# Kernel tuning notes

Hardware: AMD Instinct MI355X
Metric: run time of the kernel (lower is better)

The kernel has to match this reference:

```python
import jax, jax.numpy as jnp
import numpy as np

D = 1024
HEADS = 16
HD = D // HEADS


def setup_inputs() -> dict:
    key = jax.random.key(0)
    kx, kqkv, kout = jax.random.split(key, 3)
    x = jax.random.normal(kx, (2, 2048, D), dtype=jnp.float32)
    # torch Linear weight is [out, in]; store same layout
    W_qkv = jax.random.normal(kqkv, (3 * D, D), dtype=jnp.float32) * (D ** -0.5)
    W_out = jax.random.normal(kout, (D, D), dtype=jnp.float32) * (D ** -0.5)
    return {"x": x, "W_qkv": W_qkv, "W_out": W_out}


def reference(x, W_qkv, W_out):
    B, T, _ = x.shape
    scale = HD ** -0.5
    qkv = jnp.einsum('btd,ed->bte', x, W_qkv)            # [B,T,3D]
    qkv = qkv.reshape(B, T, 3, HEADS, HD)
    q = jnp.transpose(qkv[:, :, 0], (0, 2, 1, 3))        # [B,H,T,hd]
    k = jnp.transpose(qkv[:, :, 1], (0, 2, 1, 3))
    v = jnp.transpose(qkv[:, :, 2], (0, 2, 1, 3))
    attn = jnp.einsum('bhqd,bhkd->bhqk', q, k) * scale   # [B,H,T,T]
    causal = jnp.tril(jnp.ones((T, T), dtype=bool))
    attn = jnp.where(causal, attn, -jnp.inf)
    attn = jax.nn.softmax(attn, axis=-1)
    out = jnp.einsum('bhqk,bhkd->bhqd', attn, v)         # [B,H,T,hd]
    out = jnp.transpose(out, (0, 2, 1, 3)).reshape(B, T, HEADS * HD)
    return jnp.einsum('btd,ed->bte', out, W_out)
```

## Files before the change

### kernel.cpp

```cpp
#include <hip/hip_runtime.h>
#include <cmath>


typedef unsigned short u16;
typedef unsigned int u32;
typedef short short8 __attribute__((ext_vector_type(8)));
typedef float floatx4 __attribute__((ext_vector_type(4)));

#define T_SZ 2048
#define HD_SZ 64
#define QSCALE 0.1803368801111244f

__device__ __forceinline__ u16 f2bf(float f) {
  unsigned u = __float_as_uint(f);
  u += 0x7fffu + ((u >> 16) & 1u);
  return (u16)(u >> 16);
}

__device__ __forceinline__ u32 pack_bf2(float lo, float hi) {
  return __builtin_amdgcn_perm(__float_as_uint(hi), __float_as_uint(lo), 0x07060302u);
}

__device__ __forceinline__ void gload16(const u16* g, u16* l) {
  __builtin_amdgcn_global_load_lds(
      (const __attribute__((address_space(1))) void*)g,
      (__attribute__((address_space(3))) void*)l, 16, 0, 0);
}

__global__ __launch_bounds__(256) void cast3(const float* __restrict__ a, u16* __restrict__ ao, int na4,
                                             const float* __restrict__ b, u16* __restrict__ bo, int nb4,
                                             const float* __restrict__ c, u16* __restrict__ co, int nc4) {
  int i = blockIdx.x * 256 + threadIdx.x;
  const float* src;
  u16* dst;
  int j;
  if (i < na4) { src = a; dst = ao; j = i; }
  else if (i < na4 + nb4) { src = b; dst = bo; j = i - na4; }
  else { j = i - na4 - nb4; if (j >= nc4) return; src = c; dst = co; }
  float4 f = ((const float4*)src)[j];
  ushort4 o;
  o.x = f2bf(f.x); o.y = f2bf(f.y); o.z = f2bf(f.z); o.w = f2bf(f.w);
  ((ushort4*)dst)[j] = o;
}

__global__ __launch_bounds__(256, 3) void gemm_qkv(const u16* __restrict__ A,
                                                   const u16* __restrict__ Bt,
                                                   u16* __restrict__ Qf,
                                                   u16* __restrict__ Kf,
                                                   u16* __restrict__ Vf) {
  __shared__ u16 SM[2 * 128 * 64];
  u16* As = SM;
  u16* Bs = SM + 128 * 64;
  const int Kdim = 1024;
  const int tid = threadIdx.x;
  const int lane = tid & 63;
  const int wave = tid >> 6;
  const int quad = lane >> 4;
  const int l16 = lane & 15;
  const int wm = wave >> 1, wn = wave & 1;
  const int m0 = blockIdx.y * 128;
  const int n0 = blockIdx.x * 128;

  floatx4 acc[4][4];
#pragma unroll
  for (int i = 0; i < 4; i++)
#pragma unroll
    for (int j = 0; j < 4; j++) acc[i][j] = (floatx4){0.f, 0.f, 0.f, 0.f};

  const int srow = lane >> 3;
  const int scol = ((lane & 7) ^ srow) * 8;
  const u16* gpA[4];
  const u16* gpB[4];
  u16 *lpA[4], *lpB[4];
#pragma unroll
  for (int u = 0; u < 4; u++) {
    const int row = wave * 32 + u * 8 + srow;
    gpA[u] = A + (size_t)(m0 + row) * Kdim + scol;
    gpB[u] = Bt + (size_t)(n0 + row) * Kdim + scol;
    lpA[u] = As + (wave * 32 + u * 8) * 64 + lane * 8;
    lpB[u] = Bs + (wave * 32 + u * 8) * 64 + lane * 8;
  }

  const int fsw = l16 & 7;

  for (int k0 = 0; k0 < Kdim; k0 += 64) {
    __syncthreads();
#pragma unroll
    for (int u = 0; u < 4; u++) {
      gload16(gpA[u] + k0, lpA[u]);
      gload16(gpB[u] + k0, lpB[u]);
    }
    __syncthreads();

#pragma unroll
    for (int h = 0; h < 2; h++) {
      const int seg = ((h * 4 + quad) ^ fsw) * 8;
      short8 af[4], bf[4];
#pragma unroll
      for (int mt = 0; mt < 4; mt++)
        af[mt] = *(const short8*)&As[(wm * 64 + mt * 16 + l16) * 64 + seg];
#pragma unroll
      for (int nt = 0; nt < 4; nt++)
        bf[nt] = *(const short8*)&Bs[(wn * 64 + nt * 16 + l16) * 64 + seg];
#pragma unroll
      for (int mt = 0; mt < 4; mt++)
#pragma unroll
        for (int nt = 0; nt < 4; nt++)
          acc[mt][nt] = __builtin_amdgcn_mfma_f32_16x16x32_bf16(af[mt], bf[nt], acc[mt][nt], 0, 0, 0);
    }
  }

  const int dest = n0 >> 10;
  const int n0w = n0 + wn * 64;
  const int m_abs = m0 + wm * 64;
  const int b = m_abs >> 11;
  const int t0w = m_abs & 2047;
  const int h = (n0w >> 6) & 15;
  const int bh = b * 16 + h;
  u16* dstp = (dest == 0) ? Qf : (dest == 1) ? Kf : Vf;

  auto do_epi = [&](u16* ep) {
    if (dest == 2) {
#pragma unroll
      for (int nt = 0; nt < 4; nt++) {
#pragma unroll
        for (int mt = 0; mt < 4; mt++) {
          uint2 w;
          w.x = (u32)f2bf(acc[mt][nt][0]) | ((u32)f2bf(acc[mt][nt][1]) << 16);
          w.y = (u32)f2bf(acc[mt][nt][2]) | ((u32)f2bf(acc[mt][nt][3]) << 16);
          *(uint2*)&ep[(nt * 16 + l16) * 72 + mt * 16 + quad * 4] = w;
        }
      }
    } else {
      const float sc = (dest == 0) ? QSCALE : 1.0f;
#pragma unroll
      for (int mt = 0; mt < 4; mt++)
#pragma unroll
        for (int nt = 0; nt < 4; nt++)
#pragma unroll
          for (int r = 0; r < 4; r++)
            ep[(mt * 16 + quad * 4 + r) * 72 + nt * 16 + l16] =
                f2bf(acc[mt][nt][r] * sc);
    }
#pragma unroll
    for (int blk = 0; blk < 8; blk++) {
      const int tgd = blk >> 1;
      const int half = blk & 1;
      const short8 v = *(const short8*)&ep[(tgd * 16 + l16) * 72 + half * 32 + quad * 8];
      size_t base;
      if (dest == 0)
        base = ((size_t)(bh * 128 + (t0w >> 4) + tgd) * 2 + half) * 512;
      else
        base = (((size_t)(bh * 32 + (t0w >> 6)) * 4 + tgd) * 2 + half) * 512;
      *(short8*)(dstp + base + lane * 8) = v;
    }
  };

  __syncthreads();
  if (wave < 2) do_epi(&SM[wave * 64 * 72]);
  __syncthreads();
  if (wave >= 2) do_epi(&SM[(wave - 2) * 64 * 72]);
}

__global__ __launch_bounds__(256, 4) void gemm_out(const u16* __restrict__ A,
                                                   const u16* __restrict__ Bt,
                                                   float* __restrict__ Cout) {
  __shared__ u16 As[64 * 64];
  __shared__ u16 Bs[128 * 64];
  const int Kdim = 1024;
  const int tid = threadIdx.x;
  const int lane = tid & 63;
  const int wave = tid >> 6;
  const int quad = lane >> 4;
  const int l16 = lane & 15;
  const int wm = wave >> 1, wn = wave & 1;
  const int m0 = blockIdx.y * 64;
  const int n0 = blockIdx.x * 128;

  floatx4 acc[2][4];
#pragma unroll
  for (int i = 0; i < 2; i++)
#pragma unroll
    for (int j = 0; j < 4; j++) acc[i][j] = (floatx4){0.f, 0.f, 0.f, 0.f};

  const int srow = lane >> 3;
  const int scol = ((lane & 7) ^ srow) * 8;
  const u16* gpA[2];
  const u16* gpB[4];
  u16 *lpA[2], *lpB[4];
#pragma unroll
  for (int u = 0; u < 2; u++) {
    const int row = wave * 16 + u * 8 + srow;
    gpA[u] = A + (size_t)(m0 + row) * Kdim + scol;
    lpA[u] = As + (wave * 16 + u * 8) * 64 + lane * 8;
  }
#pragma unroll
  for (int u = 0; u < 4; u++) {
    const int row = wave * 32 + u * 8 + srow;
    gpB[u] = Bt + (size_t)(n0 + row) * Kdim + scol;
    lpB[u] = Bs + (wave * 32 + u * 8) * 64 + lane * 8;
  }

  const int fsw = l16 & 7;

  for (int k0 = 0; k0 < Kdim; k0 += 64) {
    __syncthreads();
#pragma unroll
    for (int u = 0; u < 2; u++) gload16(gpA[u] + k0, lpA[u]);
#pragma unroll
    for (int u = 0; u < 4; u++) gload16(gpB[u] + k0, lpB[u]);
    __syncthreads();

#pragma unroll
    for (int h = 0; h < 2; h++) {
      const int seg = ((h * 4 + quad) ^ fsw) * 8;
      short8 af[2], bf[4];
#pragma unroll
      for (int mt = 0; mt < 2; mt++)
        af[mt] = *(const short8*)&As[(wm * 32 + mt * 16 + l16) * 64 + seg];
#pragma unroll
      for (int nt = 0; nt < 4; nt++)
        bf[nt] = *(const short8*)&Bs[(wn * 64 + nt * 16 + l16) * 64 + seg];
#pragma unroll
      for (int mt = 0; mt < 2; mt++)
#pragma unroll
        for (int nt = 0; nt < 4; nt++)
          acc[mt][nt] = __builtin_amdgcn_mfma_f32_16x16x32_bf16(af[mt], bf[nt], acc[mt][nt], 0, 0, 0);
    }
  }

#pragma unroll
  for (int mt = 0; mt < 2; mt++)
#pragma unroll
    for (int nt = 0; nt < 4; nt++)
#pragma unroll
      for (int r = 0; r < 4; r++) {
        const int m = m0 + wm * 32 + mt * 16 + quad * 4 + r;
        const int n = n0 + wn * 64 + nt * 16 + l16;
        Cout[(size_t)m * 1024 + n] = acc[mt][nt][r];
      }
}

__global__ __launch_bounds__(256) void flash_attn(const u16* __restrict__ Qf,
                                                  const u16* __restrict__ Kf,
                                                  const u16* __restrict__ Vf,
                                                  u16* __restrict__ Og) {
  __shared__ u16 Ps[4][2][16 * 72];
  const int tid = threadIdx.x;
  const int lane = tid & 63, wave = tid >> 6;
  const int quad = lane >> 4, l16 = lane & 15;
  const int bh = blockIdx.x;
  const int py = blockIdx.y;
  const int p = (py < 8) ? py : 23 - py;
  const int gA = p, gB = 31 - p;
  const int b = bh >> 4, h = bh & 15;
  const u16* Qb = Qf + ((size_t)bh << 17);
  const u16* Kb = Kf + ((size_t)bh << 17);
  const u16* Vb = Vf + ((size_t)bh << 17);

  const u16* qpA = Qb + ((size_t)(gA * 4 + wave)) * 1024 + lane * 8;
  const u16* qpB = Qb + ((size_t)(gB * 4 + wave)) * 1024 + lane * 8;
  const short8 qfA0 = *(const short8*)qpA;
  const short8 qfA1 = *(const short8*)(qpA + 512);
  const short8 qfB0 = *(const short8*)qpB;
  const short8 qfB1 = *(const short8*)(qpB + 512);

  float lA = 0.f, lB = 0.f;
  floatx4 oA[4], oB[4];
#pragma unroll
  for (int dt = 0; dt < 4; dt++) {
    oA[dt] = (floatx4){0.f, 0.f, 0.f, 0.f};
    oB[dt] = (floatx4){0.f, 0.f, 0.f, 0.f};
  }
  u16* psA = &Ps[wave][0][0];
  u16* psB = &Ps[wave][1][0];

  short8 ka[4][2], va[4][2];

  auto stream_step = [&](bool diag, const short8& qf0, const short8& qf1,
                         floatx4* o_acc, float& l_sum, u16* ps) {
    floatx4 sacc[4];
#pragma unroll
    for (int nt = 0; nt < 4; nt++) {
      if (diag && nt > wave) continue;
      floatx4 s = (floatx4){0.f, 0.f, 0.f, 0.f};
      s = __builtin_amdgcn_mfma_f32_16x16x32_bf16(ka[nt][0], qf0, s, 0, 0, 0);
      s = __builtin_amdgcn_mfma_f32_16x16x32_bf16(ka[nt][1], qf1, s, 0, 0, 0);
      sacc[nt] = s;
    }
#pragma unroll
    for (int nt = 0; nt < 4; nt++) {
      float p0 = 0.f, p1 = 0.f, p2 = 0.f, p3 = 0.f;
      if (!(diag && nt > wave)) {
        p0 = exp2f(sacc[nt][0]);
        p1 = exp2f(sacc[nt][1]);
        p2 = exp2f(sacc[nt][2]);
        p3 = exp2f(sacc[nt][3]);
        if (diag && nt == wave) {
          if (quad * 4 + 0 > l16) p0 = 0.f;
          if (quad * 4 + 1 > l16) p1 = 0.f;
          if (quad * 4 + 2 > l16) p2 = 0.f;
          if (quad * 4 + 3 > l16) p3 = 0.f;
        }
        l_sum += (p0 + p1) + (p2 + p3);
      }
      uint2 w;
      w.x = pack_bf2(p0, p1);
      w.y = pack_bf2(p2, p3);
      *(uint2*)&ps[l16 * 72 + nt * 16 + quad * 4] = w;
    }
    const short8 pf0 = *(const short8*)&ps[l16 * 72 + quad * 8];
    const short8 pf1 = *(const short8*)&ps[l16 * 72 + 32 + quad * 8];
    const bool skip_hi = diag && (wave < 2);
#pragma unroll
    for (int dt = 0; dt < 4; dt++) {
      o_acc[dt] = __builtin_amdgcn_mfma_f32_16x16x32_bf16(va[dt][0], pf0, o_acc[dt], 0, 0, 0);
      if (!skip_hi)
        o_acc[dt] = __builtin_amdgcn_mfma_f32_16x16x32_bf16(va[dt][1], pf1, o_acc[dt], 0, 0, 0);
    }
  };

  for (int kt = 0; kt <= gB; kt++) {
    const u16* kp = Kb + (size_t)kt * 4096 + lane * 8;
    const u16* vp = Vb + (size_t)kt * 4096 + lane * 8;
#pragma unroll
    for (int nt = 0; nt < 4; nt++) {
      ka[nt][0] = *(const short8*)(kp + (nt * 2 + 0) * 512);
      ka[nt][1] = *(const short8*)(kp + (nt * 2 + 1) * 512);
    }
#pragma unroll
    for (int dt = 0; dt < 4; dt++) {
      va[dt][0] = *(const short8*)(vp + (dt * 2 + 0) * 512);
      va[dt][1] = *(const short8*)(vp + (dt * 2 + 1) * 512);
    }
    stream_step(kt == gB, qfB0, qfB1, oB, lB, psB);
    if (kt <= gA) stream_step(kt == gA, qfA0, qfA1, oA, lA, psA);
  }

  auto write_tile = [&](int g, floatx4* o_acc, float l_sum) {
    l_sum += __shfl_xor(l_sum, 16, 64);
    l_sum += __shfl_xor(l_sum, 32, 64);
    const float inv_l = 1.0f / l_sum;
    const int t0 = g * 64 + wave * 16;
    const size_t row = ((size_t)(b * 2048 + t0 + l16) << 10) + h * 64;
#pragma unroll
    for (int dt = 0; dt < 4; dt++) {
      uint2 w;
      w.x = pack_bf2(o_acc[dt][0] * inv_l, o_acc[dt][1] * inv_l);
      w.y = pack_bf2(o_acc[dt][2] * inv_l, o_acc[dt][3] * inv_l);
      *(uint2*)&Og[row + dt * 16 + quad * 4] = w;
    }
  };
  write_tile(gA, oA, lA);
  write_tile(gB, oB, lB);
}

extern "C" void kernel_launch(void* const* d_in, const int* in_sizes, int n_in,
                              void* d_out, int out_size, void* d_ws, size_t ws_size,
                              hipStream_t stream) {
  const float* x = (const float*)d_in[0];
  const float* Wqkv = (const float*)d_in[1];
  const float* Wout = (const float*)d_in[2];
  float* out = (float*)d_out;

  char* ws = (char*)d_ws;
  u16* xb    = (u16*)(ws + 0);
  u16* wqkvb = (u16*)(ws + 8388608);
  u16* woutb = (u16*)(ws + 14680064);
  u16* Qf    = (u16*)(ws + 16777216);
  u16* Kf    = (u16*)(ws + 25165824);
  u16* Vf    = (u16*)(ws + 33554432);
  u16* attn  = (u16*)(ws + 41943040);

  cast3<<<8192, 256, 0, stream>>>(x, xb, 1048576, Wqkv, wqkvb, 786432,
                                  Wout, woutb, 262144);

  gemm_qkv<<<dim3(24, 32), 256, 0, stream>>>(xb, wqkvb, Qf, Kf, Vf);

  flash_attn<<<dim3(32, 16), 256, 0, stream>>>(Qf, Kf, Vf, attn);

  gemm_out<<<dim3(8, 64), 256, 0, stream>>>(attn, woutb, out);
}
```

Before: 166.6 us.

## Split flash attention work across waves by key tiles with LDS reduction

Restructures the attention kernel so each wave handles a slice of the key dimension for all 64 query rows of a tile, rather than one 16-row query slice over all keys. Partial outputs and row sums are reduced across the four waves through shared memory before normalising and writing. The two query tiles are processed sequentially instead of interleaved, K/V are loaded once per wave per key tile, and launch bounds request two blocks per CU. This adds shared memory traffic, block-wide syncs and a cross-wave reduction epilogue, and raises register pressure from 16 output accumulators per wave.

```diff
diff --git a/kernel.cpp b/kernel.cpp
--- a/kernel.cpp
+++ b/kernel.cpp
@@ -241,118 +241,153 @@
       }
 }
 
-__global__ __launch_bounds__(256) void flash_attn(const u16* __restrict__ Qf,
-                                                  const u16* __restrict__ Kf,
-                                                  const u16* __restrict__ Vf,
-                                                  u16* __restrict__ Og) {
-  __shared__ u16 Ps[4][2][16 * 72];
+__global__ __launch_bounds__(256, 2) void flash_attn(const u16* __restrict__ Qf,
+                                                     const u16* __restrict__ Kf,
+                                                     const u16* __restrict__ Vf,
+                                                     u16* __restrict__ Og) {
+  __shared__ u16 Pq[4][4 * 16 * 40];
+  __shared__ float Osum[4][32 * 64];
+  __shared__ float Lsum[4][64];
   const int tid = threadIdx.x;
   const int lane = tid & 63, wave = tid >> 6;
   const int quad = lane >> 4, l16 = lane & 15;
   const int bh = blockIdx.x;
   const int py = blockIdx.y;
   const int p = (py < 8) ? py : 23 - py;
-  const int gA = p, gB = 31 - p;
   const int b = bh >> 4, h = bh & 15;
   const u16* Qb = Qf + ((size_t)bh << 17);
   const u16* Kb = Kf + ((size_t)bh << 17);
   const u16* Vb = Vf + ((size_t)bh << 17);
-
-  const u16* qpA = Qb + ((size_t)(gA * 4 + wave)) * 1024 + lane * 8;
-  const u16* qpB = Qb + ((size_t)(gB * 4 + wave)) * 1024 + lane * 8;
-  const short8 qfA0 = *(const short8*)qpA;
-  const short8 qfA1 = *(const short8*)(qpA + 512);
-  const short8 qfB0 = *(const short8*)qpB;
-  const short8 qfB1 = *(const short8*)(qpB + 512);
-
-  float lA = 0.f, lB = 0.f;
-  floatx4 oA[4], oB[4];
-#pragma unroll
-  for (int dt = 0; dt < 4; dt++) {
-    oA[dt] = (floatx4){0.f, 0.f, 0.f, 0.f};
-    oB[dt] = (floatx4){0.f, 0.f, 0.f, 0.f};
-  }
-  u16* psA = &Ps[wave][0][0];
-  u16* psB = &Ps[wave][1][0];
-
-  short8 ka[4][2], va[4][2];
-
-  auto stream_step = [&](bool diag, const short8& qf0, const short8& qf1,
-                         floatx4* o_acc, float& l_sum, u16* ps) {
-    floatx4 sacc[4];
-#pragma unroll
-    for (int nt = 0; nt < 4; nt++) {
-      if (diag && nt > wave) continue;
-      floatx4 s = (floatx4){0.f, 0.f, 0.f, 0.f};
-      s = __builtin_amdgcn_mfma_f32_16x16x32_bf16(ka[nt][0], qf0, s, 0, 0, 0);
-      s = __builtin_amdgcn_mfma_f32_16x16x32_bf16(ka[nt][1], qf1, s, 0, 0, 0);
-      sacc[nt] = s;
-    }
-#pragma unroll
-    for (int nt = 0; nt < 4; nt++) {
-      float p0 = 0.f, p1 = 0.f, p2 = 0.f, p3 = 0.f;
-      if (!(diag && nt > wave)) {
-        p0 = exp2f(sacc[nt][0]);
-        p1 = exp2f(sacc[nt][1]);
-        p2 = exp2f(sacc[nt][2]);
-        p3 = exp2f(sacc[nt][3]);
-        if (diag && nt == wave) {
-          if (quad * 4 + 0 > l16) p0 = 0.f;
-          if (quad * 4 + 1 > l16) p1 = 0.f;
-          if (quad * 4 + 2 > l16) p2 = 0.f;
-          if (quad * 4 + 3 > l16) p3 = 0.f;
+  u16* pq = &Pq[wave][0];
+
+  const int gs[2] = {p, 31 - p};
+
+  for (int ph = 0; ph < 2; ph++) {
+    const int g = gs[ph];
+
+    short8 qf[4][2];
+#pragma unroll
+    for (int qg = 0; qg < 4; qg++) {
+      const u16* qp = Qb + ((size_t)(g * 4 + qg)) * 1024 + lane * 8;
+      qf[qg][0] = *(const short8*)qp;
+      qf[qg][1] = *(const short8*)(qp + 512);
+    }
+
+    float l_part[4] = {0.f, 0.f, 0.f, 0.f};
+    floatx4 o[4][4];
+#pragma unroll
+    for (int dt = 0; dt < 4; dt++)
+#pragma unroll
+      for (int qg = 0; qg < 4; qg++) o[dt][qg] = (floatx4){0.f, 0.f, 0.f, 0.f};
+
+    auto process_kt = [&](int kt, int par, bool diag) {
+      const u16* kb = Kb + ((size_t)(kt * 4 + wave) * 2) * 512 + lane * 8;
+      const short8 ka0 = *(const short8*)kb;
+      const short8 ka1 = *(const short8*)(kb + 512);
+#pragma unroll
+      for (int qg = 0; qg < 4; qg++) {
+        uint2 w;
+        if (diag && wave > qg) {
+          w.x = 0u; w.y = 0u;
+        } else {
+          floatx4 s = (floatx4){0.f, 0.f, 0.f, 0.f};
+          s = __builtin_amdgcn_mfma_f32_16x16x32_bf16(ka0, qf[qg][0], s, 0, 0, 0);
+          s = __builtin_amdgcn_mfma_f32_16x16x32_bf16(ka1, qf[qg][1], s, 0, 0, 0);
+          float p0 = exp2f(s[0]);
+          float p1 = exp2f(s[1]);
+          float p2 = exp2f(s[2]);
+          float p3 = exp2f(s[3]);
+          if (diag && wave == qg) {
+            if (quad * 4 + 0 > l16) p0 = 0.f;
+            if (quad * 4 + 1 > l16) p1 = 0.f;
+            if (quad * 4 + 2 > l16) p2 = 0.f;
+            if (quad * 4 + 3 > l16) p3 = 0.f;
+          }
+          l_part[qg] += (p0 + p1) + (p2 + p3);
+          w.x = pack_bf2(p0, p1);
+          w.y = pack_bf2(p2, p3);
         }
-        l_sum += (p0 + p1) + (p2 + p3);
-      }
-      uint2 w;
-      w.x = pack_bf2(p0, p1);
-      w.y = pack_bf2(p2, p3);
-      *(uint2*)&ps[l16 * 72 + nt * 16 + quad * 4] = w;
-    }
-    const short8 pf0 = *(const short8*)&ps[l16 * 72 + quad * 8];
-    const short8 pf1 = *(const short8*)&ps[l16 * 72 + 32 + quad * 8];
-    const bool skip_hi = diag && (wave < 2);
-#pragma unroll
-    for (int dt = 0; dt < 4; dt++) {
-      o_acc[dt] = __builtin_amdgcn_mfma_f32_16x16x32_bf16(va[dt][0], pf0, o_acc[dt], 0, 0, 0);
-      if (!skip_hi)
-        o_acc[dt] = __builtin_amdgcn_mfma_f32_16x16x32_bf16(va[dt][1], pf1, o_acc[dt], 0, 0, 0);
-    }
-  };
-
-  for (int kt = 0; kt <= gB; kt++) {
-    const u16* kp = Kb + (size_t)kt * 4096 + lane * 8;
-    const u16* vp = Vb + (size_t)kt * 4096 + lane * 8;
-#pragma unroll
-    for (int nt = 0; nt < 4; nt++) {
-      ka[nt][0] = *(const short8*)(kp + (nt * 2 + 0) * 512);
-      ka[nt][1] = *(const short8*)(kp + (nt * 2 + 1) * 512);
-    }
-#pragma unroll
-    for (int dt = 0; dt < 4; dt++) {
-      va[dt][0] = *(const short8*)(vp + (dt * 2 + 0) * 512);
-      va[dt][1] = *(const short8*)(vp + (dt * 2 + 1) * 512);
-    }
-    stream_step(kt == gB, qfB0, qfB1, oB, lB, psB);
-    if (kt <= gA) stream_step(kt == gA, qfA0, qfA1, oA, lA, psA);
-  }
-
-  auto write_tile = [&](int g, floatx4* o_acc, float l_sum) {
-    l_sum += __shfl_xor(l_sum, 16, 64);
-    l_sum += __shfl_xor(l_sum, 32, 64);
-    const float inv_l = 1.0f / l_sum;
-    const int t0 = g * 64 + wave * 16;
-    const size_t row = ((size_t)(b * 2048 + t0 + l16) << 10) + h * 64;
-#pragma unroll
-    for (int dt = 0; dt < 4; dt++) {
-      uint2 w;
-      w.x = pack_bf2(o_acc[dt][0] * inv_l, o_acc[dt][1] * inv_l);
-      w.y = pack_bf2(o_acc[dt][2] * inv_l, o_acc[dt][3] * inv_l);
-      *(uint2*)&Og[row + dt * 16 + quad * 4] = w;
-    }
-  };
-  write_tile(gA, oA, lA);
-  write_tile(gB, oB, lB);
+        *(uint2*)&pq[(qg * 16 + l16) * 40 + par * 16 + quad * 4] = w;
+      }
+    };
+
+    const int npair = (g >> 1) + 1;
+    for (int ktp = 0; ktp < npair; ktp++) {
+      const int kt0 = ktp * 2;
+      const int kt1 = kt0 + 1;
+      const bool has1 = (kt1 <= g);
+
+      process_kt(kt0, 0, kt0 == g);
+      if (has1) {
+        process_kt(kt1, 1, kt1 == g);
+      } else {
+        const uint2 z = {0u, 0u};
+#pragma unroll
+        for (int qg = 0; qg < 4; qg++)
+          *(uint2*)&pq[(qg * 16 + l16) * 40 + 16 + quad * 4] = z;
+      }
+
+      short8 pf[4];
+#pragma unroll
+      for (int qg = 0; qg < 4; qg++)
+        pf[qg] = *(const short8*)&pq[(qg * 16 + l16) * 40 + quad * 8];
+
+      const int ktv = (quad < 2) ? kt0 : (has1 ? kt1 : kt0);
+      const int vl = ((wave & 1) * 2 + (quad & 1)) * 16 + l16;
+#pragma unroll
+      for (int dt = 0; dt < 4; dt++) {
+        const u16* vsrc = Vb + ((size_t)((ktv * 4 + dt) * 2 + (wave >> 1))) * 512 + vl * 8;
+        const short8 va = *(const short8*)vsrc;
+#pragma unroll
+        for (int qg = 0; qg < 4; qg++)
+          o[dt][qg] = __builtin_amdgcn_mfma_f32_16x16x32_bf16(va, pf[qg], o[dt][qg], 0, 0, 0);
+      }
+    }
+
+#pragma unroll
+    for (int qg = 0; qg < 4; qg++) {
+      l_part[qg] += __shfl_xor(l_part[qg], 16, 64);
+      l_part[qg] += __shfl_xor(l_part[qg], 32, 64);
+    }
+    if (quad == 0) {
+#pragma unroll
+      for (int qg = 0; qg < 4; qg++) Lsum[wave][qg * 16 + l16] = l_part[qg];
+    }
+
+    float linv[4];
+    for (int c = 0; c < 2; c++) {
+#pragma unroll
+      for (int dtl = 0; dtl < 2; dtl++) {
+        const int dt = c * 2 + dtl;
+#pragma unroll
+        for (int qg = 0; qg < 4; qg++)
+#pragma unroll
+          for (int r = 0; r < 4; r++)
+            Osum[wave][(dtl * 16 + quad * 4 + r) * 64 + qg * 16 + l16] = o[dt][qg][r];
+      }
+      __syncthreads();
+      if (c == 0) {
+#pragma unroll
+        for (int qg = 0; qg < 4; qg++)
+          linv[qg] = 1.0f / (Lsum[0][qg * 16 + l16] + Lsum[1][qg * 16 + l16] +
+                             Lsum[2][qg * 16 + l16] + Lsum[3][qg * 16 + l16]);
+      }
+      const int ld0 = wave * 8 + quad * 2;
+#pragma unroll
+      for (int qg = 0; qg < 4; qg++) {
+        const int qrow = qg * 16 + l16;
+        float v0 = Osum[0][(ld0 + 0) * 64 + qrow] + Osum[1][(ld0 + 0) * 64 + qrow] +
+                   Osum[2][(ld0 + 0) * 64 + qrow] + Osum[3][(ld0 + 0) * 64 + qrow];
+        float v1 = Osum[0][(ld0 + 1) * 64 + qrow] + Osum[1][(ld0 + 1) * 64 + qrow] +
+                   Osum[2][(ld0 + 1) * 64 + qrow] + Osum[3][(ld0 + 1) * 64 + qrow];
+        v0 *= linv[qg];
+        v1 *= linv[qg];
+        const size_t row = ((size_t)(b * 2048 + g * 64 + qrow) << 10) + h * 64;
+        *(u32*)&Og[row + c * 32 + ld0] = pack_bf2(v0, v1);
+      }
+      __syncthreads();
+    }
+  }
 }
 
 extern "C" void kernel_launch(void* const* d_in, const int* in_sizes, int n_in,
```

After: 167.0 us. About the same (+0.3%).
